# Kernel optimization log

Measured on AMD Instinct MI355X. Metric: run time of the kernel, lower is better.

Reference implementation:

```python
import jax, jax.numpy as jnp
import numpy as np

D = 128  # hard-coded hidden dim in MLP_T

def setup_inputs() -> dict:
    key = jax.random.key(0)
    ks = jax.random.split(key, 8)
    N, IN = 16384, 768
    return {
        "x": jax.random.normal(ks[0], (N, IN), dtype=jnp.float32),
        "decay_value": 1,
        "W_token": jax.random.normal(ks[1], (IN, D), dtype=jnp.float32) * (IN ** -0.5),
        "b_token": jax.random.normal(ks[2], (D,), dtype=jnp.float32) * 0.02,
        "W_qkv": jax.random.normal(ks[3], (D, 3 * D), dtype=jnp.float32) * (D ** -0.5),
        "b_qkv": jax.random.normal(ks[4], (3 * D,), dtype=jnp.float32) * 0.02,
        "W_fc": jax.random.normal(ks[5], (D, 1), dtype=jnp.float32) * (D ** -0.5),
        "b_fc": jax.random.normal(ks[6], (1,), dtype=jnp.float32) * 0.02,
    }

def reference(x, decay_value, W_token, b_token, W_qkv, b_qkv, W_fc, b_fc):
    # token projection: [N, in_chan] -> [N, 128]
    h = x @ W_token + b_token
    # qkv: [N, 384] split along feature dim into q, k, v of [N, 128]
    qkv = h @ W_qkv + b_qkv
    q, k, v = qkv[:, :D], qkv[:, D:2 * D], qkv[:, 2 * D:]
    # sigmoid attention (no row normalization); dropout is identity in eval mode
    att_scores = jax.nn.sigmoid(q @ k.T)            # [N, N]
    att = att_scores @ v                            # [N, 128]
    out = att @ W_fc + b_fc                         # [N, 1]
    # GradientReversal is identity in the forward pass
    return out
```

## Files before the change

### kernel.cpp

```cpp
#include <hip/hip_runtime.h>
#include <hip/hip_bf16.h>
#include <stdint.h>

#define N_ROWS 16384

typedef __bf16 bf16x8 __attribute__((ext_vector_type(8)));
typedef float f32x4 __attribute__((ext_vector_type(4)));

#define AS1 __attribute__((address_space(1)))
#define AS3 __attribute__((address_space(3)))

#define OFF_WCS  0u
#define OFF_BC   589824u
#define OFF_QB   591360u
#define OFF_KB   4785664u
#define OFF_WV   8979968u
#define OFF_PART 9045504u

__global__ void prep(const float* __restrict__ Wt, const float* __restrict__ Wq,
                     const float* __restrict__ bt, const float* __restrict__ bq,
                     __bf16* __restrict__ WcS, float* __restrict__ bc) {
    int u = blockIdx.x * 256 + threadIdx.x;
    if (u < 768 * 96) {
        int k = u / 96, n4 = u % 96;
        float s[4] = {0, 0, 0, 0};
        const float* wtp = Wt + k * 128;
        const float* wqp = Wq + n4 * 4;
#pragma unroll 8
        for (int d = 0; d < 128; d++) {
            float a = wtp[d];
            float4 b = *(const float4*)(wqp + d * 384);
            s[0] += a * b.x; s[1] += a * b.y; s[2] += a * b.z; s[3] += a * b.w;
        }
        int kb_ = k >> 6, c = (k >> 3) & 7, k7 = k & 7;
#pragma unroll
        for (int j = 0; j < 4; j++) {
            int n = n4 * 4 + j;
            WcS[n * 768 + kb_ * 64 + ((c ^ (n & 7)) << 3) + k7] = (__bf16)s[j];
        }
    }
    if (u < 384) {
        float s = bq[u];
        for (int d = 0; d < 128; d++) s += bt[d] * Wq[d * 384 + u];
        bc[u] = s;
    }
}

__launch_bounds__(256)
__global__ void gemm_qkv(const float* __restrict__ x, const __bf16* __restrict__ WcS,
                         const float* __restrict__ bc, const float* __restrict__ W_fc,
                         __bf16* __restrict__ qb, __bf16* __restrict__ kb,
                         float* __restrict__ wv) {
    __shared__ float  Asm[64 * 64];
    __shared__ __bf16 Bsm[128 * 64];
    __shared__ float  wred[64];
    const int tid = threadIdx.x, wave = tid >> 6, lane = tid & 63;
    const int n16 = lane & 15, q = lane >> 4;
    const int mh = wave >> 1, nw = wave & 1;
    const int row0 = blockIdx.x * 64;
    const int sp = blockIdx.y;

    const char* aptr[4];
    const char* bptr[4];
    {
        int p = (lane & 15) >> 1, half = lane & 1;
#pragma unroll
        for (int i = 0; i < 4; i++) {
            int ar = row0 + wave * 16 + i * 4 + (lane >> 4);
            aptr[i] = (const char*)x + (size_t)ar * 3072 + ((p ^ (ar & 7)) * 8 + half * 4) * 4;
            int br = sp * 128 + wave * 32 + i * 8 + (lane >> 3);
            bptr[i] = (const char*)WcS + (size_t)br * 1536 + (lane & 7) * 16;
        }
    }
    f32x4 acc[2][4];
#pragma unroll
    for (int mt = 0; mt < 2; mt++)
#pragma unroll
        for (int t = 0; t < 4; t++) acc[mt][t] = (f32x4){0, 0, 0, 0};

    for (int kbi = 0; kbi < 12; kbi++) {
#pragma unroll
        for (int i = 0; i < 4; i++)
            __builtin_amdgcn_global_load_lds((const AS1 void*)(aptr[i] + kbi * 256),
                (AS3 void*)((char*)Asm + wave * 4096 + i * 1024), 16, 0, 0);
#pragma unroll
        for (int i = 0; i < 4; i++)
            __builtin_amdgcn_global_load_lds((const AS1 void*)(bptr[i] + kbi * 128),
                (AS3 void*)((char*)Bsm + wave * 4096 + i * 1024), 16, 0, 0);
        __syncthreads();
#pragma unroll
        for (int ks = 0; ks < 2; ks++) {
            const int swz = ((ks * 4 + q) ^ (n16 & 7)) << 3;
            bf16x8 af[2];
#pragma unroll
            for (int mt = 0; mt < 2; mt++) {
                const float* ap = Asm + (mh * 32 + mt * 16 + n16) * 64 + swz;
                f32x4 a0 = *(const f32x4*)ap;
                f32x4 a1 = *(const f32x4*)(ap + 4);
                bf16x8 t;
                t[0] = (__bf16)a0[0]; t[1] = (__bf16)a0[1]; t[2] = (__bf16)a0[2]; t[3] = (__bf16)a0[3];
                t[4] = (__bf16)a1[0]; t[5] = (__bf16)a1[1]; t[6] = (__bf16)a1[2]; t[7] = (__bf16)a1[3];
                af[mt] = t;
            }
#pragma unroll
            for (int t = 0; t < 4; t++) {
                bf16x8 bf = *(const bf16x8*)(Bsm + (nw * 64 + t * 16 + n16) * 64 + swz);
                acc[0][t] = __builtin_amdgcn_mfma_f32_16x16x32_bf16(af[0], bf, acc[0][t], 0, 0, 0);
                acc[1][t] = __builtin_amdgcn_mfma_f32_16x16x32_bf16(af[1], bf, acc[1][t], 0, 0, 0);
            }
        }
        __syncthreads();
    }

    const int clb = nw * 64 + n16;
    if (sp == 0) {
#pragma unroll
        for (int t = 0; t < 4; t++) {
            int cl = clb + t * 16;
            float bcv = bc[cl];
#pragma unroll
            for (int mt = 0; mt < 2; mt++)
#pragma unroll
                for (int r = 0; r < 4; r++) {
                    int row = row0 + mh * 32 + mt * 16 + q * 4 + r;
                    qb[row * 128 + cl] = (__bf16)((acc[mt][t][r] + bcv) * -1.44269504088896f);
                }
        }
    } else if (sp == 1) {
#pragma unroll
        for (int t = 0; t < 4; t++) {
            int d = clb + t * 16;
            float bcv = bc[128 + d];
#pragma unroll
            for (int mt = 0; mt < 2; mt++)
#pragma unroll
                for (int r = 0; r < 4; r++) {
                    int row = row0 + mh * 32 + mt * 16 + q * 4 + r;
                    kb[row * 128 + d] = (__bf16)(acc[mt][t][r] + bcv);
                }
        }
    } else {
        float wacc[2][4] = {{0, 0, 0, 0}, {0, 0, 0, 0}};
#pragma unroll
        for (int t = 0; t < 4; t++) {
            int cl = clb + t * 16;
            float bcv = bc[256 + cl];
            float wf = W_fc[cl];
#pragma unroll
            for (int mt = 0; mt < 2; mt++)
#pragma unroll
                for (int r = 0; r < 4; r++) wacc[mt][r] += (acc[mt][t][r] + bcv) * wf;
        }
        float vred[2][4];
#pragma unroll
        for (int mt = 0; mt < 2; mt++)
#pragma unroll
            for (int r = 0; r < 4; r++) {
                float v = wacc[mt][r];
                v += __shfl_xor(v, 1, 64);
                v += __shfl_xor(v, 2, 64);
                v += __shfl_xor(v, 4, 64);
                v += __shfl_xor(v, 8, 64);
                vred[mt][r] = v;
                if (nw == 0 && n16 == 0) wred[mh * 32 + mt * 16 + q * 4 + r] = v;
            }
        __syncthreads();
        if (nw == 1 && n16 == 0) {
#pragma unroll
            for (int mt = 0; mt < 2; mt++)
#pragma unroll
                for (int r = 0; r < 4; r++) {
                    int lr = mh * 32 + mt * 16 + q * 4 + r;
                    wv[row0 + lr] = wred[lr] + vred[mt][r];
                }
        }
    }
}

__launch_bounds__(256, 4)
__global__ void attn(const __bf16* __restrict__ qb, const __bf16* __restrict__ kb,
                     const float* __restrict__ wv, float* __restrict__ partial) {
    __shared__ float red[4][64];
    const int tid = threadIdx.x;
    const int wave = tid >> 6, lane = tid & 63;
    const int n16 = lane & 15, q = lane >> 4;
    const int w_r = wave >> 1, w_k = wave & 1;

    const int lin = blockIdx.y * gridDim.x + blockIdx.x;
    const int sp = lin & 7, xb = lin >> 3;
    const int row0 = xb * 128 + w_r * 64;
    const int jbase = sp * 2048 + w_k * 1024;

    bf16x8 qf[4][4];
#pragma unroll
    for (int mt = 0; mt < 4; mt++)
#pragma unroll
        for (int ks = 0; ks < 4; ks++)
            qf[mt][ks] = *(const bf16x8*)(qb + (size_t)(row0 + mt * 16 + n16) * 128 + ks * 32 + q * 8);

    float acc[4][4] = {{0}, {0}, {0}, {0}};

    const __bf16* kp = kb + (size_t)(jbase + n16) * 128 + q * 8;
    const float* wp = wv + jbase + n16;

    for (int t = 0; t < 64; t++) {
        bf16x8 bf[4];
#pragma unroll
        for (int ks = 0; ks < 4; ks++)
            bf[ks] = *(const bf16x8*)(kp + (size_t)t * 16 * 128 + ks * 32);
        float wval = wp[t * 16];

        f32x4 s[4];
#pragma unroll
        for (int mt = 0; mt < 4; mt++) s[mt] = (f32x4){0, 0, 0, 0};
#pragma unroll
        for (int ks = 0; ks < 4; ks++) {
#pragma unroll
            for (int mt = 0; mt < 4; mt++)
                s[mt] = __builtin_amdgcn_mfma_f32_16x16x32_bf16(qf[mt][ks], bf[ks], s[mt], 0, 0, 0);
        }
#pragma unroll
        for (int mt = 0; mt < 4; mt++)
#pragma unroll
            for (int r = 0; r < 4; r++)
                acc[mt][r] += __builtin_amdgcn_rcpf(1.0f + __builtin_amdgcn_exp2f(s[mt][r])) * wval;
    }

#pragma unroll
    for (int mt = 0; mt < 4; mt++)
#pragma unroll
        for (int r = 0; r < 4; r++) {
            float v = acc[mt][r];
            v += __shfl_xor(v, 1, 64);
            v += __shfl_xor(v, 2, 64);
            v += __shfl_xor(v, 4, 64);
            v += __shfl_xor(v, 8, 64);
            if (n16 == 0) red[wave][mt * 16 + q * 4 + r] = v;
        }
    __syncthreads();
    if (tid < 128) {
        int g = tid >> 6, l = tid & 63;
        partial[sp * N_ROWS + xb * 128 + g * 64 + l] = red[g * 2][l] + red[g * 2 + 1][l];
    }
}

__global__ void reduce_out(const float* __restrict__ partial, const float* __restrict__ b_fc,
                           float* __restrict__ out) {
    int i = blockIdx.x * 256 + threadIdx.x;
    float v = b_fc[0];
#pragma unroll
    for (int s = 0; s < 8; s++) v += partial[s * N_ROWS + i];
    out[i] = v;
}

extern "C" void kernel_launch(void* const* d_in, const int* in_sizes, int n_in,
                              void* d_out, int out_size, void* d_ws, size_t ws_size,
                              hipStream_t stream) {
    const float* x       = (const float*)d_in[0];
    const float* W_token = (const float*)d_in[2];
    const float* b_token = (const float*)d_in[3];
    const float* W_qkv   = (const float*)d_in[4];
    const float* b_qkv   = (const float*)d_in[5];
    const float* W_fc    = (const float*)d_in[6];
    const float* b_fc    = (const float*)d_in[7];
    float* out = (float*)d_out;
    char* ws = (char*)d_ws;

    __bf16* WcS = (__bf16*)(ws + OFF_WCS);
    float*  bc  = (float*)(ws + OFF_BC);
    __bf16* qb  = (__bf16*)(ws + OFF_QB);
    __bf16* kb  = (__bf16*)(ws + OFF_KB);
    float*  wv  = (float*)(ws + OFF_WV);
    float*  part = (float*)(ws + OFF_PART);

    prep<<<288, 256, 0, stream>>>(W_token, W_qkv, b_token, b_qkv, WcS, bc);
    gemm_qkv<<<dim3(256, 3), 256, 0, stream>>>(x, WcS, bc, W_fc, qb, kb, wv);
    attn<<<dim3(128, 8), 256, 0, stream>>>(qb, kb, wv, part);
    reduce_out<<<64, 256, 0, stream>>>(part, b_fc, out);
}
```

Before: 248.6 us.

## Stream K tiles into per-wave LDS rings via async global_load_lds with software pipelining

The attention kernel now copies K and wv tiles straight from global memory into a per-wave 4-slot LDS ring using global_load_lds, prefetching two chunks ahead. The K layout in global memory is XOR-swizzled so the LDS reads avoid bank conflicts. The sigmoid epilogue of one chunk is interleaved with the MFMAs of the next through double-buffered score registers, with setprio raised around the MFMAs. The work split also changes from 128-row blocks to 64-row blocks with each wave covering a distinct key range, so 2048 blocks are launched. The cost is about 74KB of LDS per block, which limits occupancy to 2 blocks per CU, and the Q fragments are now reloaded twice as often overall.

```diff
diff --git a/kernel.cpp b/kernel.cpp
--- a/kernel.cpp
+++ b/kernel.cpp
@@ -136,7 +136,7 @@
 #pragma unroll
                 for (int r = 0; r < 4; r++) {
                     int row = row0 + mh * 32 + mt * 16 + q * 4 + r;
-                    kb[row * 128 + d] = (__bf16)(acc[mt][t][r] + bcv);
+                    kb[row * 128 + (((d >> 3) ^ (row & 15)) << 3) + (d & 7)] = (__bf16)(acc[mt][t][r] + bcv);
                 }
         }
     } else {
@@ -177,19 +177,22 @@
     }
 }
 
-__launch_bounds__(256, 4)
+__launch_bounds__(256, 2)
 __global__ void attn(const __bf16* __restrict__ qb, const __bf16* __restrict__ kb,
                      const float* __restrict__ wv, float* __restrict__ partial) {
-    __shared__ float red[4][64];
+    __shared__ __align__(16) char smem[75776];
     const int tid = threadIdx.x;
     const int wave = tid >> 6, lane = tid & 63;
     const int n16 = lane & 15, q = lane >> 4;
-    const int w_r = wave >> 1, w_k = wave & 1;
-
-    const int lin = blockIdx.y * gridDim.x + blockIdx.x;
-    const int sp = lin & 7, xb = lin >> 3;
-    const int row0 = xb * 128 + w_r * 64;
-    const int jbase = sp * 2048 + w_k * 1024;
+    const int bid = blockIdx.x;
+    const int sp = bid & 7;
+    const int qbi = bid >> 3;
+    const int row0 = qbi * 64;
+    const int kbase = sp * 2048 + wave * 512;
+
+    char* myring = smem + wave * 16384;
+    float* mywv = (float*)(smem + 65536 + wave * 2048);
+    float* redbuf = (float*)(smem + 73728);
 
     bf16x8 qf[4][4];
 #pragma unroll
@@ -197,33 +200,85 @@
 #pragma unroll
         for (int ks = 0; ks < 4; ks++)
             qf[mt][ks] = *(const bf16x8*)(qb + (size_t)(row0 + mt * 16 + n16) * 128 + ks * 32 + q * 8);
+    __builtin_amdgcn_sched_barrier(0);
+
+    {
+        const char* wsrc = (const char*)(wv + kbase) + lane * 16;
+        __builtin_amdgcn_global_load_lds((const AS1 void*)wsrc, (AS3 void*)((char*)mywv + lane * 16 - lane * 16 + lane * 16), 16, 0, 0);
+    }
+    __builtin_amdgcn_global_load_lds((const AS1 void*)((const char*)(wv + kbase) + 1024 + lane * 16),
+                                     (AS3 void*)((char*)mywv + 1024), 16, 0, 0);
+
+#define ISSUE(c, slot)                                                                   \
+    {                                                                                    \
+        const char* g = (const char*)kb + (size_t)(kbase + (c) * 16) * 256 + lane * 16;  \
+        char* d = myring + (slot) * 4096;                                                \
+        __builtin_amdgcn_global_load_lds((const AS1 void*)g,          (AS3 void*)d,          16, 0, 0); \
+        __builtin_amdgcn_global_load_lds((const AS1 void*)(g + 1024), (AS3 void*)(d + 1024), 16, 0, 0); \
+        __builtin_amdgcn_global_load_lds((const AS1 void*)(g + 2048), (AS3 void*)(d + 2048), 16, 0, 0); \
+        __builtin_amdgcn_global_load_lds((const AS1 void*)(g + 3072), (AS3 void*)(d + 3072), 16, 0, 0); \
+    }
+
+    ISSUE(0, 0);
+    ISSUE(1, 1);
 
     float acc[4][4] = {{0}, {0}, {0}, {0}};
-
-    const __bf16* kp = kb + (size_t)(jbase + n16) * 128 + q * 8;
-    const float* wp = wv + jbase + n16;
-
-    for (int t = 0; t < 64; t++) {
-        bf16x8 bf[4];
-#pragma unroll
-        for (int ks = 0; ks < 4; ks++)
-            bf[ks] = *(const bf16x8*)(kp + (size_t)t * 16 * 128 + ks * 32);
-        float wval = wp[t * 16];
-
-        f32x4 s[4];
-#pragma unroll
-        for (int mt = 0; mt < 4; mt++) s[mt] = (f32x4){0, 0, 0, 0};
-#pragma unroll
-        for (int ks = 0; ks < 4; ks++) {
-#pragma unroll
-            for (int mt = 0; mt < 4; mt++)
-                s[mt] = __builtin_amdgcn_mfma_f32_16x16x32_bf16(qf[mt][ks], bf[ks], s[mt], 0, 0, 0);
-        }
-#pragma unroll
-        for (int mt = 0; mt < 4; mt++)
-#pragma unroll
-            for (int r = 0; r < 4; r++)
-                acc[mt][r] += __builtin_amdgcn_rcpf(1.0f + __builtin_amdgcn_exp2f(s[mt][r])) * wval;
+    f32x4 psA0 = (f32x4){0,0,0,0}, psA1 = (f32x4){0,0,0,0}, psA2 = (f32x4){0,0,0,0}, psA3 = (f32x4){0,0,0,0};
+    f32x4 psB0 = (f32x4){0,0,0,0}, psB1 = (f32x4){0,0,0,0}, psB2 = (f32x4){0,0,0,0}, psB3 = (f32x4){0,0,0,0};
+    float pw = 0.0f;
+
+    const char* kaddr[4];
+#pragma unroll
+    for (int ks = 0; ks < 4; ks++)
+        kaddr[ks] = myring + n16 * 256 + (((ks * 4 + q) ^ n16) << 4);
+    const float* wbase = mywv + n16;
+
+#define STEP(W0, W1, W2, W3, R0, R1, R2, R3, OFFB, WCUR)                                 \
+    {                                                                                    \
+        W0 = (f32x4){0,0,0,0}; W1 = (f32x4){0,0,0,0};                                    \
+        W2 = (f32x4){0,0,0,0}; W3 = (f32x4){0,0,0,0};                                    \
+        __builtin_amdgcn_s_setprio(1);                                                   \
+        _Pragma("unroll")                                                                \
+        for (int ks = 0; ks < 4; ks++) {                                                 \
+            bf16x8 bf = *(const bf16x8*)(kaddr[ks] + (OFFB));                            \
+            W0 = __builtin_amdgcn_mfma_f32_16x16x32_bf16(qf[0][ks], bf, W0, 0, 0, 0);    \
+            W1 = __builtin_amdgcn_mfma_f32_16x16x32_bf16(qf[1][ks], bf, W1, 0, 0, 0);    \
+            W2 = __builtin_amdgcn_mfma_f32_16x16x32_bf16(qf[2][ks], bf, W2, 0, 0, 0);    \
+            W3 = __builtin_amdgcn_mfma_f32_16x16x32_bf16(qf[3][ks], bf, W3, 0, 0, 0);    \
+        }                                                                                \
+        __builtin_amdgcn_s_setprio(0);                                                   \
+        _Pragma("unroll")                                                                \
+        for (int r = 0; r < 4; r++) {                                                    \
+            acc[0][r] += __builtin_amdgcn_rcpf(1.0f + __builtin_amdgcn_exp2f(R0[r])) * pw; \
+            acc[1][r] += __builtin_amdgcn_rcpf(1.0f + __builtin_amdgcn_exp2f(R1[r])) * pw; \
+            acc[2][r] += __builtin_amdgcn_rcpf(1.0f + __builtin_amdgcn_exp2f(R2[r])) * pw; \
+            acc[3][r] += __builtin_amdgcn_rcpf(1.0f + __builtin_amdgcn_exp2f(R3[r])) * pw; \
+        }                                                                                \
+        pw = (WCUR);                                                                     \
+    }
+
+#pragma unroll 4
+    for (int c = 0; c < 32; c++) {
+        const int cn = (c + 2 < 32) ? c + 2 : 31;
+        ISSUE(cn, (c + 2) & 3);
+        asm volatile("s_waitcnt vmcnt(8)" ::: "memory");
+        __builtin_amdgcn_sched_barrier(0);
+        const int sb = (c & 3) * 4096;
+        if ((c & 1) == 0) {
+            STEP(psA0, psA1, psA2, psA3, psB0, psB1, psB2, psB3, sb, wbase[c * 16]);
+        } else {
+            STEP(psB0, psB1, psB2, psB3, psA0, psA1, psA2, psA3, sb, wbase[c * 16]);
+        }
+    }
+#undef STEP
+#undef ISSUE
+
+#pragma unroll
+    for (int r = 0; r < 4; r++) {
+        acc[0][r] += __builtin_amdgcn_rcpf(1.0f + __builtin_amdgcn_exp2f(psB0[r])) * pw;
+        acc[1][r] += __builtin_amdgcn_rcpf(1.0f + __builtin_amdgcn_exp2f(psB1[r])) * pw;
+        acc[2][r] += __builtin_amdgcn_rcpf(1.0f + __builtin_amdgcn_exp2f(psB2[r])) * pw;
+        acc[3][r] += __builtin_amdgcn_rcpf(1.0f + __builtin_amdgcn_exp2f(psB3[r])) * pw;
     }
 
 #pragma unroll
@@ -235,12 +290,12 @@
             v += __shfl_xor(v, 2, 64);
             v += __shfl_xor(v, 4, 64);
             v += __shfl_xor(v, 8, 64);
-            if (n16 == 0) red[wave][mt * 16 + q * 4 + r] = v;
+            if (n16 == 0) redbuf[wave * 64 + mt * 16 + q * 4 + r] = v;
         }
     __syncthreads();
-    if (tid < 128) {
-        int g = tid >> 6, l = tid & 63;
-        partial[sp * N_ROWS + xb * 128 + g * 64 + l] = red[g * 2][l] + red[g * 2 + 1][l];
+    if (tid < 64) {
+        float s = redbuf[tid] + redbuf[64 + tid] + redbuf[128 + tid] + redbuf[192 + tid];
+        partial[sp * N_ROWS + row0 + tid] = s;
     }
 }
 
@@ -275,6 +330,6 @@
 
     prep<<<288, 256, 0, stream>>>(W_token, W_qkv, b_token, b_qkv, WcS, bc);
     gemm_qkv<<<dim3(256, 3), 256, 0, stream>>>(x, WcS, bc, W_fc, qb, kb, wv);
-    attn<<<dim3(128, 8), 256, 0, stream>>>(qb, kb, wv, part);
+    attn<<<2048, 256, 0, stream>>>(qb, kb, wv, part);
     reduce_out<<<64, 256, 0, stream>>>(part, b_fc, out);
 }
```

Result: faster. 211.7 us (-14.8%).
